# Optimization experiments

Hardware: AMD Instinct MI355X
Metric: run time of the kernel (lower is better)

## Reference

```python
import jax, jax.numpy as jnp
import numpy as np

T, O, K = 256, 64, 16
H, W = 224, 224
D_MODEL, D_OBJ = 768, 2048
GAMMA_INIT = 0.1
OMEGA = 1e-06


def setup_inputs() -> dict:
    key = jax.random.key(0)
    ks = jax.random.split(key, 8)
    obj_feat = jax.random.normal(ks[0], (T, O, D_OBJ), dtype=jnp.float32)
    frame_feat = jax.random.normal(ks[1], (T, D_MODEL), dtype=jnp.float32)
    mark_embeddings = jax.random.normal(ks[2], (K, D_MODEL), dtype=jnp.float32)
    obj_entity = jax.random.randint(ks[3], (T, O), 0, K + 1, dtype=jnp.int32)
    masks = jax.random.randint(ks[4], (T, H, W), 0, K + 1, dtype=jnp.int32)
    # learned params (nn.Linear: y = x @ W.T + b; here stored as [in, out])
    W_obj = jax.random.normal(ks[5], (D_MODEL, D_OBJ), dtype=jnp.float32) / np.sqrt(D_MODEL)
    b_obj = jnp.zeros((D_OBJ,), dtype=jnp.float32)
    W_frame = jax.random.normal(ks[6], (D_MODEL, D_MODEL), dtype=jnp.float32) / np.sqrt(D_MODEL)
    b_frame = jnp.zeros((D_MODEL,), dtype=jnp.float32)
    gamma = jnp.asarray(GAMMA_INIT, dtype=jnp.float32)
    return {
        "obj_feat": obj_feat,
        "frame_feat": frame_feat,
        "mark_embeddings": mark_embeddings,
        "obj_entity": obj_entity,
        "masks": masks,
        "W_obj": W_obj,
        "b_obj": b_obj,
        "W_frame": W_frame,
        "b_frame": b_frame,
        "gamma": gamma,
    }


def reference(obj_feat, frame_feat, mark_embeddings, obj_entity, masks,
              W_obj, b_obj, W_frame, b_frame, gamma):
    # ---- inject_objects: o_hat = o + gamma * P_obj(r_k) (Eq. 4.2) ----
    proj_obj = mark_embeddings @ W_obj + b_obj            # [K, D_OBJ]
    valid = (obj_entity > 0)                              # entity_id == 0 -> no mark
    idx = jnp.clip(obj_entity - 1, 0)                     # [T, O]
    obj_out = obj_feat + gamma * jnp.where(valid[..., None], proj_obj[idx], 0.0)

    # ---- inject_frames: S_t = sum_k (m_k * r_k) / (omega + sum_k m_k) (Eq. 4.3) ----
    Tn, Kn = frame_feat.shape[0], mark_embeddings.shape[0]
    flat = masks.reshape(Tn, -1)                          # [T, H*W]
    seg = (flat + (Kn + 1) * jnp.arange(Tn, dtype=flat.dtype)[:, None]).reshape(-1)
    counts = jax.ops.segment_sum(
        jnp.ones(seg.shape, dtype=jnp.float32), seg, num_segments=Tn * (Kn + 1)
    ).reshape(Tn, Kn + 1)[:, 1:]                          # [T, K] pixel counts per entity
    proj_frame = mark_embeddings @ W_frame + b_frame      # [K, d_model]
    spatial = counts @ proj_frame                         # [T, d_model]
    weight = OMEGA + counts.sum(axis=-1, keepdims=True)   # [T, 1]
    frame_out = frame_feat + gamma * spatial / weight

    return obj_out, frame_out
```

## Files before the change

kernel.cpp:

```cpp
#include <hip/hip_runtime.h>

#define T_N 256
#define O_N 64
#define K_N 16
#define HW_N (224 * 224)
#define DM 768
#define DO 2048
#define OMEGA_F 1e-6f

#define PCOLS 64
#define DSEG 64
#define NSEG (DM / DSEG)
#define NT_O (DO / PCOLS)
#define NT_F (DM / PCOLS)
#define NB_PROJ ((NT_O + NT_F) * NSEG)
#define SUBB 4
#define NB_HIST (T_N * SUBB)

#define NB_OBJ (T_N * O_N / 4)

__global__ __launch_bounds__(256) void fusedA(const float* __restrict__ me,
                                              const float* __restrict__ Wo, const float* __restrict__ bo,
                                              const float* __restrict__ Wf, const float* __restrict__ bf,
                                              const int* __restrict__ masks,
                                              float* __restrict__ proj_obj, float* __restrict__ proj_frame,
                                              float* __restrict__ counts_partial) {
    __shared__ char smem[20480];
    const int b = blockIdx.x;
    const int tid = threadIdx.x;

    if (b < NB_PROJ) {
        float (*partial)[K_N][PCOLS] = (float (*)[K_N][PCOLS])smem;
        float* me_s = (float*)(smem + 4 * K_N * PCOLS * sizeof(float));
        const int tile = b / NSEG, seg = b - tile * NSEG;
        const float* W; const float* bias; float* out; int ld; int j0;
        if (tile < NT_O) { W = Wo; bias = bo; out = proj_obj;   ld = DO; j0 = tile * PCOLS; }
        else             { W = Wf; bias = bf; out = proj_frame; ld = DM; j0 = (tile - NT_O) * PCOLS; }
        const int d0 = seg * DSEG;

        for (int i = tid; i < K_N * DSEG; i += 256) {
            int k = i >> 6, dd = i & 63;
            me_s[i] = me[k * DM + d0 + dd];
        }
        __syncthreads();

        const int jj = tid & (PCOLS - 1);
        const int s  = tid >> 6;
        const int j  = j0 + jj;
        const int db = s * 16;

        float acc[K_N];
        #pragma unroll
        for (int k = 0; k < K_N; ++k) acc[k] = 0.f;

        #pragma unroll
        for (int dd = 0; dd < 16; ++dd) {
            float w = W[(size_t)(d0 + db + dd) * ld + j];
            #pragma unroll
            for (int k = 0; k < K_N; ++k)
                acc[k] += me_s[k * DSEG + db + dd] * w;
        }
        #pragma unroll
        for (int k = 0; k < K_N; ++k) partial[s][k][jj] = acc[k];
        __syncthreads();

        for (int o = tid; o < K_N * PCOLS; o += 256) {
            int k = o >> 6, c = o & 63;
            float v = partial[0][k][c] + partial[1][k][c]
                    + partial[2][k][c] + partial[3][k][c];
            if (seg == NSEG - 1) v += bias[j0 + c];
            atomicAdd(&out[k * ld + j0 + c], v);
        }
    } else {
        int* bins = (int*)smem;
        int (*partial2)[17] = (int (*)[17])(smem + 256 * 17 * 4);
        const int hb = b - NB_PROJ;
        const int t = hb >> 2, sub = hb & 3;
        int* my = &bins[tid * 17];
        #pragma unroll
        for (int i = 0; i < 17; ++i) my[i] = 0;

        const int4* p = (const int4*)(masks + (size_t)t * HW_N);
        const int n4 = HW_N / 4;
        const int chunk = n4 / SUBB;
        const int end = (sub + 1) * chunk;
        for (int i = sub * chunk + tid; i < end; i += 256) {
            int4 v = p[i];
            my[v.x]++; my[v.y]++; my[v.z]++; my[v.w]++;
        }
        __syncthreads();
        const int bcol = tid & 15, rg = tid >> 4;
        int ssum = 0;
        #pragma unroll
        for (int r = 0; r < 16; ++r) ssum += bins[(rg * 16 + r) * 17 + (bcol + 1)];
        partial2[rg][bcol] = ssum;
        __syncthreads();
        if (tid < 16) {
            int s = 0;
            #pragma unroll
            for (int r = 0; r < 16; ++r) s += partial2[r][tid];
            counts_partial[((size_t)sub * T_N + t) * K_N + tid] = (float)s;
        }
    }
}

__global__ __launch_bounds__(256) void fusedB(const float* __restrict__ obj_feat,
                                              const int* __restrict__ obj_entity,
                                              const float* __restrict__ proj_obj,
                                              const float* __restrict__ frame_feat,
                                              const float* __restrict__ counts_partial,
                                              const float* __restrict__ proj_frame,
                                              const float* __restrict__ gamma,
                                              float* __restrict__ obj_out,
                                              float* __restrict__ frame_out) {
    __shared__ float c[K_N];
    const int b = blockIdx.x;
    const float g = gamma[0];

    if (b < NB_OBJ) {
        const int wave = threadIdx.x >> 6;
        const int lane = threadIdx.x & 63;
        const int row = b * 4 + wave;
        const int e = obj_entity[row];
        const float4* __restrict__ src = (const float4*)(obj_feat + (size_t)row * DO);
        float4* __restrict__ dst = (float4*)(obj_out + (size_t)row * DO);
        if (e > 0) {
            const float4* __restrict__ pr = (const float4*)(proj_obj + (size_t)(e - 1) * DO);
            float4 a[8], p[8];
            #pragma unroll
            for (int it = 0; it < 8; ++it) a[it] = src[lane + it * 64];
            #pragma unroll
            for (int it = 0; it < 8; ++it) p[it] = pr[lane + it * 64];
            #pragma unroll
            for (int it = 0; it < 8; ++it)
                dst[lane + it * 64] = make_float4(a[it].x + g * p[it].x,
                                                  a[it].y + g * p[it].y,
                                                  a[it].z + g * p[it].z,
                                                  a[it].w + g * p[it].w);
        } else {
            float4 a[8];
            #pragma unroll
            for (int it = 0; it < 8; ++it) a[it] = src[lane + it * 64];
            #pragma unroll
            for (int it = 0; it < 8; ++it) dst[lane + it * 64] = a[it];
        }
    } else {
        const int t = b - NB_OBJ;
        if (threadIdx.x < K_N) {
            float s = 0.f;
            #pragma unroll
            for (int sb = 0; sb < SUBB; ++sb)
                s += counts_partial[((size_t)sb * T_N + t) * K_N + threadIdx.x];
            c[threadIdx.x] = s;
        }
        __syncthreads();
        float tot = 0.f;
        #pragma unroll
        for (int k = 0; k < K_N; ++k) tot += c[k];
        const float inv = g / (OMEGA_F + tot);
        for (int j = threadIdx.x; j < DM; j += 256) {
            float acc = 0.f;
            #pragma unroll
            for (int k = 0; k < K_N; ++k) acc += c[k] * proj_frame[k * DM + j];
            frame_out[t * DM + j] = frame_feat[t * DM + j] + acc * inv;
        }
    }
}

extern "C" void kernel_launch(void* const* d_in, const int* in_sizes, int n_in,
                              void* d_out, int out_size, void* d_ws, size_t ws_size,
                              hipStream_t stream) {
    const float* obj_feat   = (const float*)d_in[0];
    const float* frame_feat = (const float*)d_in[1];
    const float* me         = (const float*)d_in[2];
    const int*   obj_entity = (const int*)d_in[3];
    const int*   masks      = (const int*)d_in[4];
    const float* Wo         = (const float*)d_in[5];
    const float* bo         = (const float*)d_in[6];
    const float* Wf         = (const float*)d_in[7];
    const float* bf         = (const float*)d_in[8];
    const float* gamma      = (const float*)d_in[9];

    float* obj_out   = (float*)d_out;
    float* frame_out = (float*)d_out + (size_t)T_N * O_N * DO;

    float* ws = (float*)d_ws;
    float* proj_obj       = ws;
    float* proj_frame     = ws + 32768;
    float* counts_partial = ws + 32768 + 12288;

    hipMemsetAsync(ws, 0, (size_t)(32768 + 12288) * sizeof(float), stream);

    fusedA<<<NB_PROJ + NB_HIST, 256, 0, stream>>>(
        me, Wo, bo, Wf, bf, masks, proj_obj, proj_frame, counts_partial);
    fusedB<<<NB_OBJ + T_N, 256, 0, stream>>>(
        obj_feat, obj_entity, proj_obj, frame_feat, counts_partial, proj_frame,
        gamma, obj_out, frame_out);
}
```

Baseline: 79.31 us.

## Regroup kernels so histogram overlaps object injection, add nontemporal stores

```diff
diff --git a/kernel.cpp b/kernel.cpp
--- a/kernel.cpp
+++ b/kernel.cpp
@@ -8,6 +8,8 @@
 #define DO 2048
 #define OMEGA_F 1e-6f
 
+typedef float f32x4 __attribute__((ext_vector_type(4)));
+
 #define PCOLS 64
 #define DSEG 64
 #define NSEG (DM / DSEG)
@@ -16,66 +18,73 @@
 #define NB_PROJ ((NT_O + NT_F) * NSEG)
 #define SUBB 4
 #define NB_HIST (T_N * SUBB)
-
 #define NB_OBJ (T_N * O_N / 4)
 
-__global__ __launch_bounds__(256) void fusedA(const float* __restrict__ me,
-                                              const float* __restrict__ Wo, const float* __restrict__ bo,
-                                              const float* __restrict__ Wf, const float* __restrict__ bf,
-                                              const int* __restrict__ masks,
-                                              float* __restrict__ proj_obj, float* __restrict__ proj_frame,
-                                              float* __restrict__ counts_partial) {
-    __shared__ char smem[20480];
+__global__ __launch_bounds__(256) void proj_kernel(const float* __restrict__ me,
+                                                   const float* __restrict__ Wo, const float* __restrict__ bo,
+                                                   const float* __restrict__ Wf, const float* __restrict__ bf,
+                                                   float* __restrict__ proj_obj, float* __restrict__ proj_frame) {
+    __shared__ float partial[4][K_N][PCOLS];
+    __shared__ float me_s[K_N * DSEG];
     const int b = blockIdx.x;
     const int tid = threadIdx.x;
 
-    if (b < NB_PROJ) {
-        float (*partial)[K_N][PCOLS] = (float (*)[K_N][PCOLS])smem;
-        float* me_s = (float*)(smem + 4 * K_N * PCOLS * sizeof(float));
-        const int tile = b / NSEG, seg = b - tile * NSEG;
-        const float* W; const float* bias; float* out; int ld; int j0;
-        if (tile < NT_O) { W = Wo; bias = bo; out = proj_obj;   ld = DO; j0 = tile * PCOLS; }
-        else             { W = Wf; bias = bf; out = proj_frame; ld = DM; j0 = (tile - NT_O) * PCOLS; }
-        const int d0 = seg * DSEG;
+    const int tile = b / NSEG, seg = b - tile * NSEG;
+    const float* W; const float* bias; float* out; int ld; int j0;
+    if (tile < NT_O) { W = Wo; bias = bo; out = proj_obj;   ld = DO; j0 = tile * PCOLS; }
+    else             { W = Wf; bias = bf; out = proj_frame; ld = DM; j0 = (tile - NT_O) * PCOLS; }
+    const int d0 = seg * DSEG;
 
-        for (int i = tid; i < K_N * DSEG; i += 256) {
-            int k = i >> 6, dd = i & 63;
-            me_s[i] = me[k * DM + d0 + dd];
-        }
-        __syncthreads();
+    for (int i = tid; i < K_N * DSEG; i += 256) {
+        int k = i >> 6, dd = i & 63;
+        me_s[i] = me[k * DM + d0 + dd];
+    }
+    __syncthreads();
 
-        const int jj = tid & (PCOLS - 1);
-        const int s  = tid >> 6;
-        const int j  = j0 + jj;
-        const int db = s * 16;
+    const int jj = tid & (PCOLS - 1);
+    const int s  = tid >> 6;
+    const int j  = j0 + jj;
+    const int db = s * 16;
 
-        float acc[K_N];
+    float acc[K_N];
+    #pragma unroll
+    for (int k = 0; k < K_N; ++k) acc[k] = 0.f;
+
+    #pragma unroll
+    for (int dd = 0; dd < 16; ++dd) {
+        float w = W[(size_t)(d0 + db + dd) * ld + j];
         #pragma unroll
-        for (int k = 0; k < K_N; ++k) acc[k] = 0.f;
+        for (int k = 0; k < K_N; ++k)
+            acc[k] += me_s[k * DSEG + db + dd] * w;
+    }
+    #pragma unroll
+    for (int k = 0; k < K_N; ++k) partial[s][k][jj] = acc[k];
+    __syncthreads();
 
-        #pragma unroll
-        for (int dd = 0; dd < 16; ++dd) {
-            float w = W[(size_t)(d0 + db + dd) * ld + j];
-            #pragma unroll
-            for (int k = 0; k < K_N; ++k)
-                acc[k] += me_s[k * DSEG + db + dd] * w;
-        }
-        #pragma unroll
-        for (int k = 0; k < K_N; ++k) partial[s][k][jj] = acc[k];
-        __syncthreads();
+    for (int o = tid; o < K_N * PCOLS; o += 256) {
+        int k = o >> 6, c = o & 63;
+        float v = partial[0][k][c] + partial[1][k][c]
+                + partial[2][k][c] + partial[3][k][c];
+        if (seg == NSEG - 1) v += bias[j0 + c];
+        atomicAdd(&out[k * ld + j0 + c], v);
+    }
+}
 
-        for (int o = tid; o < K_N * PCOLS; o += 256) {
-            int k = o >> 6, c = o & 63;
-            float v = partial[0][k][c] + partial[1][k][c]
-                    + partial[2][k][c] + partial[3][k][c];
-            if (seg == NSEG - 1) v += bias[j0 + c];
-            atomicAdd(&out[k * ld + j0 + c], v);
-        }
-    } else {
+__global__ __launch_bounds__(256) void objhist_kernel(const int* __restrict__ masks,
+                                                      float* __restrict__ counts_partial,
+                                                      const float* __restrict__ obj_feat,
+                                                      const int* __restrict__ obj_entity,
+                                                      const float* __restrict__ proj_obj,
+                                                      const float* __restrict__ gamma,
+                                                      float* __restrict__ obj_out) {
+    __shared__ char smem[18496];
+    const int b = blockIdx.x;
+    const int tid = threadIdx.x;
+
+    if (b < NB_HIST) {
         int* bins = (int*)smem;
         int (*partial2)[17] = (int (*)[17])(smem + 256 * 17 * 4);
-        const int hb = b - NB_PROJ;
-        const int t = hb >> 2, sub = hb & 3;
+        const int t = b >> 2, sub = b & 3;
         int* my = &bins[tid * 17];
         #pragma unroll
         for (int i = 0; i < 17; ++i) my[i] = 0;
@@ -101,69 +110,61 @@
             for (int r = 0; r < 16; ++r) s += partial2[r][tid];
             counts_partial[((size_t)sub * T_N + t) * K_N + tid] = (float)s;
         }
-    }
-}
-
-__global__ __launch_bounds__(256) void fusedB(const float* __restrict__ obj_feat,
-                                              const int* __restrict__ obj_entity,
-                                              const float* __restrict__ proj_obj,
-                                              const float* __restrict__ frame_feat,
-                                              const float* __restrict__ counts_partial,
-                                              const float* __restrict__ proj_frame,
-                                              const float* __restrict__ gamma,
-                                              float* __restrict__ obj_out,
-                                              float* __restrict__ frame_out) {
-    __shared__ float c[K_N];
-    const int b = blockIdx.x;
-    const float g = gamma[0];
-
-    if (b < NB_OBJ) {
-        const int wave = threadIdx.x >> 6;
-        const int lane = threadIdx.x & 63;
-        const int row = b * 4 + wave;
+    } else {
+        const int wave = tid >> 6;
+        const int lane = tid & 63;
+        const int row = (b - NB_HIST) * 4 + wave;
         const int e = obj_entity[row];
-        const float4* __restrict__ src = (const float4*)(obj_feat + (size_t)row * DO);
-        float4* __restrict__ dst = (float4*)(obj_out + (size_t)row * DO);
+        const float g = gamma[0];
+        const f32x4* __restrict__ src = (const f32x4*)(obj_feat + (size_t)row * DO);
+        f32x4* __restrict__ dst = (f32x4*)(obj_out + (size_t)row * DO);
         if (e > 0) {
-            const float4* __restrict__ pr = (const float4*)(proj_obj + (size_t)(e - 1) * DO);
-            float4 a[8], p[8];
+            const f32x4* __restrict__ pr = (const f32x4*)(proj_obj + (size_t)(e - 1) * DO);
+            f32x4 a[8], p[8];
             #pragma unroll
             for (int it = 0; it < 8; ++it) a[it] = src[lane + it * 64];
             #pragma unroll
             for (int it = 0; it < 8; ++it) p[it] = pr[lane + it * 64];
             #pragma unroll
-            for (int it = 0; it < 8; ++it)
-                dst[lane + it * 64] = make_float4(a[it].x + g * p[it].x,
-                                                  a[it].y + g * p[it].y,
-                                                  a[it].z + g * p[it].z,
-                                                  a[it].w + g * p[it].w);
+            for (int it = 0; it < 8; ++it) {
+                f32x4 r = a[it] + g * p[it];
+                __builtin_nontemporal_store(r, &dst[lane + it * 64]);
+            }
         } else {
-            float4 a[8];
             #pragma unroll
-            for (int it = 0; it < 8; ++it) a[it] = src[lane + it * 64];
-            #pragma unroll
-            for (int it = 0; it < 8; ++it) dst[lane + it * 64] = a[it];
+            for (int it = 0; it < 8; ++it) {
+                f32x4 a = src[lane + it * 64];
+                __builtin_nontemporal_store(a, &dst[lane + it * 64]);
+            }
         }
-    } else {
-        const int t = b - NB_OBJ;
-        if (threadIdx.x < K_N) {
-            float s = 0.f;
-            #pragma unroll
-            for (int sb = 0; sb < SUBB; ++sb)
-                s += counts_partial[((size_t)sb * T_N + t) * K_N + threadIdx.x];
-            c[threadIdx.x] = s;
-        }
-        __syncthreads();
-        float tot = 0.f;
+    }
+}
+
+__global__ __launch_bounds__(256) void frame_kernel(const float* __restrict__ frame_feat,
+                                                    const float* __restrict__ counts_partial,
+                                                    const float* __restrict__ proj_frame,
+                                                    const float* __restrict__ gamma,
+                                                    float* __restrict__ frame_out) {
+    __shared__ float c[K_N];
+    const int t = blockIdx.x;
+    const float g = gamma[0];
+    if (threadIdx.x < K_N) {
+        float s = 0.f;
         #pragma unroll
-        for (int k = 0; k < K_N; ++k) tot += c[k];
-        const float inv = g / (OMEGA_F + tot);
-        for (int j = threadIdx.x; j < DM; j += 256) {
-            float acc = 0.f;
-            #pragma unroll
-            for (int k = 0; k < K_N; ++k) acc += c[k] * proj_frame[k * DM + j];
-            frame_out[t * DM + j] = frame_feat[t * DM + j] + acc * inv;
-        }
+        for (int sb = 0; sb < SUBB; ++sb)
+            s += counts_partial[((size_t)sb * T_N + t) * K_N + threadIdx.x];
+        c[threadIdx.x] = s;
+    }
+    __syncthreads();
+    float tot = 0.f;
+    #pragma unroll
+    for (int k = 0; k < K_N; ++k) tot += c[k];
+    const float inv = g / (OMEGA_F + tot);
+    for (int j = threadIdx.x; j < DM; j += 256) {
+        float acc = 0.f;
+        #pragma unroll
+        for (int k = 0; k < K_N; ++k) acc += c[k] * proj_frame[k * DM + j];
+        frame_out[t * DM + j] = frame_feat[t * DM + j] + acc * inv;
     }
 }
 
@@ -191,9 +192,8 @@
 
     hipMemsetAsync(ws, 0, (size_t)(32768 + 12288) * sizeof(float), stream);
 
-    fusedA<<<NB_PROJ + NB_HIST, 256, 0, stream>>>(
-        me, Wo, bo, Wf, bf, masks, proj_obj, proj_frame, counts_partial);
-    fusedB<<<NB_OBJ + T_N, 256, 0, stream>>>(
-        obj_feat, obj_entity, proj_obj, frame_feat, counts_partial, proj_frame,
-        gamma, obj_out, frame_out);
+    proj_kernel<<<NB_PROJ, 256, 0, stream>>>(me, Wo, bo, Wf, bf, proj_obj, proj_frame);
+    objhist_kernel<<<NB_HIST + NB_OBJ, 256, 0, stream>>>(
+        masks, counts_partial, obj_feat, obj_entity, proj_obj, gamma, obj_out);
+    frame_kernel<<<T_N, 256, 0, stream>>>(frame_feat, counts_partial, proj_frame, gamma, frame_out);
 }
```

New measurement: 67.51 us. 14.9% less time.
